# Optimization experiments

Measured on AMD Instinct MI355X. Metric: run time of the kernel, lower is better.

Reference implementation:

```python
import jax, jax.numpy as jnp
import numpy as np

B, N, C, H, W = 8, 64, 256, 100, 100
PROJ_C, HID, EMB = 256, 128, 64
GN_EPS = 1e-5
NORM_EPS = 1e-6


def setup_inputs() -> dict:
    key = jax.random.key(0)
    ks = jax.random.split(key, 8)
    features = jax.random.normal(ks[0], (B, C, H, W), dtype=jnp.float32)
    boxes_xyxy = jax.random.uniform(ks[1], (B, N, 4), dtype=jnp.float32)  # normalized boxes in [0,1]
    conv_w = jax.random.normal(ks[2], (PROJ_C, C), dtype=jnp.float32) * (1.0 / np.sqrt(C))  # 1x1 conv, no bias
    gn_w = jnp.ones((PROJ_C,), dtype=jnp.float32)
    gn_b = jnp.zeros((PROJ_C,), dtype=jnp.float32)
    w1 = jax.random.normal(ks[3], (PROJ_C, HID), dtype=jnp.float32) * (1.0 / np.sqrt(PROJ_C))
    b1 = jnp.zeros((HID,), dtype=jnp.float32)
    w2 = jax.random.normal(ks[4], (HID, EMB), dtype=jnp.float32) * (1.0 / np.sqrt(HID))
    b2 = jnp.zeros((EMB,), dtype=jnp.float32)
    return {"features": features, "boxes_xyxy": boxes_xyxy, "conv_w": conv_w,
            "gn_w": gn_w, "gn_b": gn_b, "w1": w1, "b1": b1, "w2": w2, "b2": b2}


def _silu(x):
    return x * jax.nn.sigmoid(x)


def _forward(features, boxes_xyxy, conv_w, gn_w, gn_b, w1, b1, w2, b2):
    # feature_proj: 1x1 conv (no bias) -> GroupNorm(groups=1) -> SiLU
    y = jnp.einsum('bchw,oc->bohw', features, conv_w)
    mu = y.mean(axis=(1, 2, 3), keepdims=True)
    var = y.var(axis=(1, 2, 3), keepdims=True)
    y = (y - mu) * jax.lax.rsqrt(var + GN_EPS)
    y = y * gn_w[None, :, None, None] + gn_b[None, :, None, None]
    src = _silu(y)  # [B,PROJ_C,H,W]

    # project normalized boxes to feature coords (normalized_boxes=True)
    x1 = jnp.minimum(boxes_xyxy[..., 0], boxes_xyxy[..., 2]) * W
    x2 = jnp.maximum(boxes_xyxy[..., 0], boxes_xyxy[..., 2]) * W
    y1 = jnp.minimum(boxes_xyxy[..., 1], boxes_xyxy[..., 3]) * H
    y2 = jnp.maximum(boxes_xyxy[..., 1], boxes_xyxy[..., 3]) * H
    x1 = jnp.clip(jnp.floor(jnp.clip(x1, 0.0, W)), 0.0, W)
    x2 = jnp.clip(jnp.ceil(jnp.clip(x2, 0.0, W)), 0.0, W)
    y1 = jnp.clip(jnp.floor(jnp.clip(y1, 0.0, H)), 0.0, H)
    y2 = jnp.clip(jnp.ceil(jnp.clip(y2, 0.0, H)), 0.0, H)

    # separable region masks: region is rows y1:y2, cols x1:x2
    hs = jnp.arange(H, dtype=jnp.float32)
    ws = jnp.arange(W, dtype=jnp.float32)
    my = ((hs >= y1[..., None]) & (hs < y2[..., None])).astype(src.dtype)  # [B,N,H]
    mx = ((ws >= x1[..., None]) & (ws < x2[..., None])).astype(src.dtype)  # [B,N,W]

    region_sum = jnp.einsum('bnh,bnw,bchw->bnc', my, mx, src)
    count = my.sum(-1) * mx.sum(-1)  # [B,N]
    pooled = jnp.where(count[..., None] > 0, region_sum / jnp.maximum(count[..., None], 1.0), 0.0)

    # embedding MLP + L2 normalize (torch F.normalize semantics)
    raw = _silu(pooled @ w1 + b1) @ w2 + b2
    norm = jnp.linalg.norm(raw, axis=-1, keepdims=True)
    emb = raw / jnp.maximum(norm, NORM_EPS)
    return emb, raw, pooled


def reference(features, boxes_xyxy, conv_w, gn_w, gn_b, w1, b1, w2, b2):
    return _forward(features, boxes_xyxy, conv_w, gn_w, gn_b, w1, b1, w2, b2)
```

## Files before the change

kernel.cpp:

```cpp
#include <hip/hip_runtime.h>
#include <math.h>

#define HWq 10000
#define Cq 256
#define Oq 256

typedef __attribute__((ext_vector_type(8))) short short8v;
typedef __attribute__((ext_vector_type(4))) float f32x4;

__device__ __forceinline__ short f2bf(float f) {
    unsigned u = __float_as_uint(f);
    return (short)((u + 0x7FFFu + ((u >> 16) & 1u)) >> 16);
}
__device__ __forceinline__ float bf2f(unsigned short u) {
    return __uint_as_float((unsigned)u << 16);
}

__device__ __forceinline__ int swz(int row, int g) {
    return g ^ (row & 3) ^ ((row >> 2) & 1);
}

__global__ __launch_bounds__(256) void conv_mfma(const float* __restrict__ feat,
                                                 const float* __restrict__ convw,
                                                 unsigned short* __restrict__ y,
                                                 float* __restrict__ stats) {
    __shared__ __align__(16) short Al[2][128 * 32];
    __shared__ __align__(16) short Bl[2][128 * 32];
    __shared__ float redbuf[8];

    const int b  = blockIdx.z;
    const int o0 = blockIdx.y * 128;
    const int p0 = blockIdx.x * 128;
    const int t  = threadIdx.x;
    const int w  = t >> 6;
    const int l  = t & 63;
    const int wo = (w >> 1) * 64;
    const int wp = (w & 1) * 64;

    const float* fb = feat + (size_t)b * Cq * HWq;

    f32x4 acc[4][4];
    #pragma unroll
    for (int i = 0; i < 4; ++i)
        #pragma unroll
        for (int j = 0; j < 4; ++j)
            acc[i][j] = (f32x4){0.f, 0.f, 0.f, 0.f};

    const int oA0 = t >> 2;
    const int oA1 = oA0 + 64;
    const int kuA = t & 3;
    const float* aptr0 = convw + (size_t)(o0 + oA0) * Cq + kuA * 8;
    const float* aptr1 = convw + (size_t)(o0 + oA1) * Cq + kuA * 8;

    int pgB[2];
    #pragma unroll
    for (int pass = 0; pass < 2; ++pass) {
        int pg = p0 + pass * 64 + l;
        pgB[pass] = (pg > HWq - 1) ? (HWq - 1) : pg;
    }

    const int fr_g = l >> 4;
    const int fr_r = l & 15;

    float4 ra0, ra1, ra2, ra3;
    float  rb[2][8];

    auto LOADG = [&](int k0) {
        ra0 = *(const float4*)(aptr0 + k0);
        ra1 = *(const float4*)(aptr0 + k0 + 4);
        ra2 = *(const float4*)(aptr1 + k0);
        ra3 = *(const float4*)(aptr1 + k0 + 4);
        #pragma unroll
        for (int pass = 0; pass < 2; ++pass) {
            const float* fk = fb + (size_t)(k0 + w * 8) * HWq + pgB[pass];
            #pragma unroll
            for (int jj = 0; jj < 8; ++jj)
                rb[pass][jj] = fk[(size_t)jj * HWq];
        }
    };

    auto WRITE = [&](int bi) {
        short8v s;
        s[0]=f2bf(ra0.x); s[1]=f2bf(ra0.y); s[2]=f2bf(ra0.z); s[3]=f2bf(ra0.w);
        s[4]=f2bf(ra1.x); s[5]=f2bf(ra1.y); s[6]=f2bf(ra1.z); s[7]=f2bf(ra1.w);
        *(short8v*)((char*)Al[bi] + oA0 * 64 + swz(oA0, kuA) * 16) = s;
        short8v s2;
        s2[0]=f2bf(ra2.x); s2[1]=f2bf(ra2.y); s2[2]=f2bf(ra2.z); s2[3]=f2bf(ra2.w);
        s2[4]=f2bf(ra3.x); s2[5]=f2bf(ra3.y); s2[6]=f2bf(ra3.z); s2[7]=f2bf(ra3.w);
        *(short8v*)((char*)Al[bi] + oA1 * 64 + swz(oA1, kuA) * 16) = s2;
        #pragma unroll
        for (int pass = 0; pass < 2; ++pass) {
            short8v sb;
            #pragma unroll
            for (int jj = 0; jj < 8; ++jj) sb[jj] = f2bf(rb[pass][jj]);
            int p = pass * 64 + l;
            *(short8v*)((char*)Bl[bi] + p * 64 + swz(p, w) * 16) = sb;
        }
    };

    LOADG(0);
    WRITE(0);
    LOADG(32);
    __syncthreads();

    int cur = 0;
    for (int k0 = 0; k0 < Cq; k0 += 32) {
        short8v af[4], bfv[4];
        #pragma unroll
        for (int i = 0; i < 4; ++i) {
            int row = wo + i * 16 + fr_r;
            af[i] = *(const short8v*)((const char*)Al[cur] + row * 64 + swz(row, fr_g) * 16);
        }
        #pragma unroll
        for (int j = 0; j < 4; ++j) {
            int row = wp + j * 16 + fr_r;
            bfv[j] = *(const short8v*)((const char*)Bl[cur] + row * 64 + swz(row, fr_g) * 16);
        }
        if (k0 + 32 < Cq) {
            WRITE(cur ^ 1);
            if (k0 + 64 < Cq) LOADG(k0 + 64);
        }
        #pragma unroll
        for (int i = 0; i < 4; ++i)
            #pragma unroll
            for (int j = 0; j < 4; ++j)
                acc[i][j] = __builtin_amdgcn_mfma_f32_16x16x32_bf16(af[i], bfv[j], acc[i][j], 0, 0, 0);
        __syncthreads();
        cur ^= 1;
    }

    float lsum = 0.f, lsq = 0.f;
    #pragma unroll
    for (int i = 0; i < 4; ++i) {
        const int obase = o0 + wo + i * 16 + (l >> 4) * 4;
        #pragma unroll
        for (int j = 0; j < 4; ++j) {
            const int p = p0 + wp + j * 16 + (l & 15);
            if (p < HWq) {
                #pragma unroll
                for (int r = 0; r < 4; ++r) {
                    float v = acc[i][j][r];
                    y[((size_t)(b * Oq + obase + r)) * HWq + p] = (unsigned short)f2bf(v);
                    lsum += v;
                    lsq  += v * v;
                }
            }
        }
    }
    #pragma unroll
    for (int m = 1; m < 64; m <<= 1) {
        lsum += __shfl_xor(lsum, m);
        lsq  += __shfl_xor(lsq, m);
    }
    if (l == 0) { redbuf[w] = lsum; redbuf[4 + w] = lsq; }
    __syncthreads();
    if (t == 0) {
        atomicAdd(&stats[b],     redbuf[0] + redbuf[1] + redbuf[2] + redbuf[3]);
        atomicAdd(&stats[8 + b], redbuf[4] + redbuf[5] + redbuf[6] + redbuf[7]);
    }
}

__global__ __launch_bounds__(256) void integral_pool(const unsigned short* __restrict__ y,
                                                     const float* __restrict__ boxes,
                                                     const float* __restrict__ stats,
                                                     const float* __restrict__ gnw,
                                                     const float* __restrict__ gnb,
                                                     float* __restrict__ pooled) {
    __shared__ float Sl[10000];

    const int plane = blockIdx.x;
    const int b = plane >> 8;
    const int c = plane & 255;
    const int wave = threadIdx.x >> 6;
    const int lane = threadIdx.x & 63;

    const float invM = 1.f / 2560000.f;
    const float mu   = stats[b] * invM;
    const float msq  = stats[8 + b] * invM;
    const float rs   = rsqrtf(msq - mu * mu + 1e-5f);
    const float scale = gnw[c] * rs;
    const float shift = gnb[c] - mu * scale;

    const unsigned short* yp = y + (size_t)plane * HWq;

    for (int i = 0; i < 25; i += 2) {
        const int r0 = wave + 4 * i;
        const int r1 = r0 + 4;
        const bool has1 = (i + 1) < 25;
        float a0 = 0.f, b0 = 0.f, a1 = 0.f, b1 = 0.f;
        if (lane < 50) {
            ushort2 u0 = *(const ushort2*)(yp + r0 * 100 + 2 * lane);
            float v0 = bf2f(u0.x) * scale + shift;
            float v1 = bf2f(u0.y) * scale + shift;
            a0 = v0 / (1.f + __expf(-v0));
            b0 = v1 / (1.f + __expf(-v1));
            if (has1) {
                ushort2 u1 = *(const ushort2*)(yp + r1 * 100 + 2 * lane);
                float w0 = bf2f(u1.x) * scale + shift;
                float w1 = bf2f(u1.y) * scale + shift;
                a1 = w0 / (1.f + __expf(-w0));
                b1 = w1 / (1.f + __expf(-w1));
            }
        }
        float p0 = a0 + b0;
        float p1 = a1 + b1;
        #pragma unroll
        for (int m = 1; m < 64; m <<= 1) {
            float t0 = __shfl_up(p0, m);
            float t1 = __shfl_up(p1, m);
            if (lane >= m) { p0 += t0; p1 += t1; }
        }
        if (lane < 50) {
            float2 o0 = {p0 - b0, p0};
            *(float2*)(&Sl[r0 * 100 + 2 * lane]) = o0;
            if (has1) {
                float2 o1 = {p1 - b1, p1};
                *(float2*)(&Sl[r1 * 100 + 2 * lane]) = o1;
            }
        }
    }
    __syncthreads();

    {
        const int grp = lane >> 2;
        const int j   = lane & 3;
        const int n   = wave * 16 + grp;
        const float4 bx = *(const float4*)(boxes + ((size_t)b * 64 + n) * 4);

        float x1f = fminf(bx.x, bx.z) * 100.f;
        float x2f = fmaxf(bx.x, bx.z) * 100.f;
        float y1f = fminf(bx.y, bx.w) * 100.f;
        float y2f = fmaxf(bx.y, bx.w) * 100.f;
        x1f = fminf(fmaxf(floorf(fminf(fmaxf(x1f, 0.f), 100.f)), 0.f), 100.f);
        x2f = fminf(fmaxf(ceilf (fminf(fmaxf(x2f, 0.f), 100.f)), 0.f), 100.f);
        y1f = fminf(fmaxf(floorf(fminf(fmaxf(y1f, 0.f), 100.f)), 0.f), 100.f);
        y2f = fminf(fmaxf(ceilf (fminf(fmaxf(y2f, 0.f), 100.f)), 0.f), 100.f);
        const int ix1 = (int)x1f, ix2 = (int)x2f;
        const int iy1 = (int)y1f, iy2 = (int)y2f;
        const int cnt = (ix2 - ix1) * (iy2 - iy1);

        float v = 0.f;
        if (cnt > 0) {
            const int colR = ix2 - 1;
            const int colL = ix1 - 1;
            for (int h = iy1 + j; h < iy2; h += 4) {
                float s = Sl[h * 100 + colR];
                if (colL >= 0) s -= Sl[h * 100 + colL];
                v += s;
            }
        }
        v += __shfl_xor(v, 1);
        v += __shfl_xor(v, 2);
        if (j == 0)
            pooled[((size_t)b * 64 + n) * Cq + c] = (cnt > 0) ? v / (float)cnt : 0.f;
    }
}

__global__ __launch_bounds__(128) void mlp_kernel(const float* __restrict__ pooled,
                                                  const float* __restrict__ w1,
                                                  const float* __restrict__ b1,
                                                  const float* __restrict__ w2,
                                                  const float* __restrict__ b2,
                                                  float* __restrict__ emb,
                                                  float* __restrict__ raw) {
    __shared__ float ps[256];
    __shared__ float hs[128];
    const int bn = blockIdx.x;
    const int t  = threadIdx.x;

    ps[t]       = pooled[(size_t)bn * 256 + t];
    ps[t + 128] = pooled[(size_t)bn * 256 + t + 128];
    __syncthreads();

    float a = b1[t];
    #pragma unroll 8
    for (int c = 0; c < 256; ++c) a += ps[c] * w1[c * 128 + t];
    hs[t] = a / (1.f + __expf(-a));
    __syncthreads();

    if (t < 64) {
        float r = b2[t];
        #pragma unroll 8
        for (int h = 0; h < 128; ++h) r += hs[h] * w2[h * 64 + t];
        raw[(size_t)bn * 64 + t] = r;
        float s = r * r;
        #pragma unroll
        for (int m = 1; m < 64; m <<= 1) s += __shfl_xor(s, m);
        float nrm = fmaxf(sqrtf(s), 1e-6f);
        emb[(size_t)bn * 64 + t] = r / nrm;
    }
}

extern "C" void kernel_launch(void* const* d_in, const int* in_sizes, int n_in,
                              void* d_out, int out_size, void* d_ws, size_t ws_size,
                              hipStream_t stream) {
    const float* feat  = (const float*)d_in[0];
    const float* boxes = (const float*)d_in[1];
    const float* convw = (const float*)d_in[2];
    const float* gnw   = (const float*)d_in[3];
    const float* gnb   = (const float*)d_in[4];
    const float* w1    = (const float*)d_in[5];
    const float* b1    = (const float*)d_in[6];
    const float* w2    = (const float*)d_in[7];
    const float* b2    = (const float*)d_in[8];

    float* out    = (float*)d_out;
    float* emb    = out;
    float* raw    = out + 32768;
    float* pooled = out + 65536;

    unsigned short* y = (unsigned short*)d_ws;
    float* stats = (float*)((char*)d_ws + (size_t)8 * 256 * 10000 * 2);

    hipMemsetAsync(stats, 0, 16 * sizeof(float), stream);

    dim3 g1((HWq + 127) / 128, 2, 8);
    conv_mfma<<<g1, 256, 0, stream>>>(feat, convw, y, stats);

    integral_pool<<<2048, 256, 0, stream>>>(y, boxes, stats, gnw, gnb, pooled);

    mlp_kernel<<<512, 128, 0, stream>>>(pooled, w1, b1, w2, b2, emb, raw);
}
```

Measured before the change: 230.3 us.

## Switch conv GEMM to single LDS buffer and split MLP accumulators

The conv GEMM drops its double-buffered shared-memory staging for a single buffer. Each iteration now converts and writes the tile, synchronizes, issues the next global loads and then runs the MFMAs. This halves LDS use and may allow more blocks per CU, but it adds a second barrier per k-step and less overlap between the LDS writes and compute. The bf16 conversion now uses the HIP intrinsic, and the MLP dot products use four independent accumulators to shorten dependency chains.

Result: faster. 216.8 us (-5.8%).

```diff
diff --git a/kernel.cpp b/kernel.cpp
--- a/kernel.cpp
+++ b/kernel.cpp
@@ -1,4 +1,5 @@
 #include <hip/hip_runtime.h>
+#include <hip/hip_bf16.h>
 #include <math.h>
 
 #define HWq 10000
@@ -9,8 +10,8 @@
 typedef __attribute__((ext_vector_type(4))) float f32x4;
 
 __device__ __forceinline__ short f2bf(float f) {
-    unsigned u = __float_as_uint(f);
-    return (short)((u + 0x7FFFu + ((u >> 16) & 1u)) >> 16);
+    __hip_bfloat16 h = __float2bfloat16(f);
+    return *reinterpret_cast<short*>(&h);
 }
 __device__ __forceinline__ float bf2f(unsigned short u) {
     return __uint_as_float((unsigned)u << 16);
@@ -24,8 +25,8 @@
                                                  const float* __restrict__ convw,
                                                  unsigned short* __restrict__ y,
                                                  float* __restrict__ stats) {
-    __shared__ __align__(16) short Al[2][128 * 32];
-    __shared__ __align__(16) short Bl[2][128 * 32];
+    __shared__ __align__(16) short Albuf[128 * 32];
+    __shared__ __align__(16) short Blbuf[128 * 32];
     __shared__ float redbuf[8];
 
     const int b  = blockIdx.z;
@@ -79,54 +80,49 @@
         }
     };
 
-    auto WRITE = [&](int bi) {
-        short8v s;
-        s[0]=f2bf(ra0.x); s[1]=f2bf(ra0.y); s[2]=f2bf(ra0.z); s[3]=f2bf(ra0.w);
-        s[4]=f2bf(ra1.x); s[5]=f2bf(ra1.y); s[6]=f2bf(ra1.z); s[7]=f2bf(ra1.w);
-        *(short8v*)((char*)Al[bi] + oA0 * 64 + swz(oA0, kuA) * 16) = s;
-        short8v s2;
-        s2[0]=f2bf(ra2.x); s2[1]=f2bf(ra2.y); s2[2]=f2bf(ra2.z); s2[3]=f2bf(ra2.w);
-        s2[4]=f2bf(ra3.x); s2[5]=f2bf(ra3.y); s2[6]=f2bf(ra3.z); s2[7]=f2bf(ra3.w);
-        *(short8v*)((char*)Al[bi] + oA1 * 64 + swz(oA1, kuA) * 16) = s2;
-        #pragma unroll
-        for (int pass = 0; pass < 2; ++pass) {
-            short8v sb;
+    LOADG(0);
+
+    for (int k0 = 0; k0 < Cq; k0 += 32) {
+        if (k0) __syncthreads();
+
+        {
+            short8v s;
+            s[0]=f2bf(ra0.x); s[1]=f2bf(ra0.y); s[2]=f2bf(ra0.z); s[3]=f2bf(ra0.w);
+            s[4]=f2bf(ra1.x); s[5]=f2bf(ra1.y); s[6]=f2bf(ra1.z); s[7]=f2bf(ra1.w);
+            *(short8v*)((char*)Albuf + oA0 * 64 + swz(oA0, kuA) * 16) = s;
+            short8v s2;
+            s2[0]=f2bf(ra2.x); s2[1]=f2bf(ra2.y); s2[2]=f2bf(ra2.z); s2[3]=f2bf(ra2.w);
+            s2[4]=f2bf(ra3.x); s2[5]=f2bf(ra3.y); s2[6]=f2bf(ra3.z); s2[7]=f2bf(ra3.w);
+            *(short8v*)((char*)Albuf + oA1 * 64 + swz(oA1, kuA) * 16) = s2;
             #pragma unroll
-            for (int jj = 0; jj < 8; ++jj) sb[jj] = f2bf(rb[pass][jj]);
-            int p = pass * 64 + l;
-            *(short8v*)((char*)Bl[bi] + p * 64 + swz(p, w) * 16) = sb;
-        }
-    };
-
-    LOADG(0);
-    WRITE(0);
-    LOADG(32);
-    __syncthreads();
-
-    int cur = 0;
-    for (int k0 = 0; k0 < Cq; k0 += 32) {
+            for (int pass = 0; pass < 2; ++pass) {
+                short8v sb;
+                #pragma unroll
+                for (int jj = 0; jj < 8; ++jj) sb[jj] = f2bf(rb[pass][jj]);
+                int p = pass * 64 + l;
+                *(short8v*)((char*)Blbuf + p * 64 + swz(p, w) * 16) = sb;
+            }
+        }
+        __syncthreads();
+
+        if (k0 < Cq - 32) LOADG(k0 + 32);
+
         short8v af[4], bfv[4];
         #pragma unroll
         for (int i = 0; i < 4; ++i) {
             int row = wo + i * 16 + fr_r;
-            af[i] = *(const short8v*)((const char*)Al[cur] + row * 64 + swz(row, fr_g) * 16);
+            af[i] = *(const short8v*)((const char*)Albuf + row * 64 + swz(row, fr_g) * 16);
         }
         #pragma unroll
         for (int j = 0; j < 4; ++j) {
             int row = wp + j * 16 + fr_r;
-            bfv[j] = *(const short8v*)((const char*)Bl[cur] + row * 64 + swz(row, fr_g) * 16);
-        }
-        if (k0 + 32 < Cq) {
-            WRITE(cur ^ 1);
-            if (k0 + 64 < Cq) LOADG(k0 + 64);
+            bfv[j] = *(const short8v*)((const char*)Blbuf + row * 64 + swz(row, fr_g) * 16);
         }
         #pragma unroll
         for (int i = 0; i < 4; ++i)
             #pragma unroll
             for (int j = 0; j < 4; ++j)
                 acc[i][j] = __builtin_amdgcn_mfma_f32_16x16x32_bf16(af[i], bfv[j], acc[i][j], 0, 0, 0);
-        __syncthreads();
-        cur ^= 1;
     }
 
     float lsum = 0.f, lsq = 0.f;
@@ -272,16 +268,28 @@
     ps[t + 128] = pooled[(size_t)bn * 256 + t + 128];
     __syncthreads();
 
-    float a = b1[t];
-    #pragma unroll 8
-    for (int c = 0; c < 256; ++c) a += ps[c] * w1[c * 128 + t];
+    float a0 = 0.f, a1 = 0.f, a2 = 0.f, a3 = 0.f;
+    #pragma unroll 4
+    for (int c = 0; c < 256; c += 4) {
+        a0 += ps[c]     * w1[c * 128 + t];
+        a1 += ps[c + 1] * w1[(c + 1) * 128 + t];
+        a2 += ps[c + 2] * w1[(c + 2) * 128 + t];
+        a3 += ps[c + 3] * w1[(c + 3) * 128 + t];
+    }
+    float a = b1[t] + ((a0 + a1) + (a2 + a3));
     hs[t] = a / (1.f + __expf(-a));
     __syncthreads();
 
     if (t < 64) {
-        float r = b2[t];
-        #pragma unroll 8
-        for (int h = 0; h < 128; ++h) r += hs[h] * w2[h * 64 + t];
+        float r0 = 0.f, r1 = 0.f, r2 = 0.f, r3 = 0.f;
+        #pragma unroll 4
+        for (int h = 0; h < 128; h += 4) {
+            r0 += hs[h]     * w2[h * 64 + t];
+            r1 += hs[h + 1] * w2[(h + 1) * 64 + t];
+            r2 += hs[h + 2] * w2[(h + 2) * 64 + t];
+            r3 += hs[h + 3] * w2[(h + 3) * 64 + t];
+        }
+        float r = b2[t] + ((r0 + r1) + (r2 + r3));
         raw[(size_t)bn * 64 + t] = r;
         float s = r * r;
         #pragma unroll
```
